# Kernel tuning notes

Measured on AMD Instinct MI355X. Metric: run time of the kernel, lower is better.

## Reference

```python
import jax, jax.numpy as jnp
import numpy as np

N = 8192
IN_DIM = 128
HID = 32


def setup_inputs() -> dict:
    key = jax.random.key(0)
    ks = jax.random.split(key, 8)
    x = jax.random.normal(ks[0], (N, IN_DIM), dtype=jnp.float32)
    adj = jax.random.uniform(ks[1], (N, N), dtype=jnp.float32)
    # Linear params (torch nn.Linear: y = x @ W.T + b); store as [in, out] for einsum.
    def lin(k, fan_in, fan_out):
        bound = 1.0 / np.sqrt(fan_in)
        kw, kb = jax.random.split(k)
        W = jax.random.uniform(kw, (fan_in, fan_out), minval=-bound, maxval=bound, dtype=jnp.float32)
        b = jax.random.uniform(kb, (fan_out,), minval=-bound, maxval=bound, dtype=jnp.float32)
        return W, b
    W1, b1 = lin(ks[2], IN_DIM, HID)
    W2, b2 = lin(ks[3], HID, HID)
    W3, b3 = lin(ks[4], HID, 1)
    return {"x": x, "adj": adj, "W1": W1, "b1": b1, "W2": W2, "b2": b2, "W3": W3, "b3": b3}


def reference(x, adj, W1, b1, W2, b2, W3, b3):
    # a_hat = adj + I (self loops)
    n = adj.shape[0]
    a_hat = adj + jnp.eye(n, dtype=adj.dtype)
    degree = jnp.sum(a_hat, axis=1)
    d_inv_sqrt = jnp.clip(degree, 1.0, None) ** -0.5  # [N]
    # D^-1/2 A D^-1/2 as row/col scaling (same math as diag matmuls, no O(N^3) waste)
    a_norm = d_inv_sqrt[:, None] * a_hat * d_inv_sqrt[None, :]
    h = jax.nn.relu(a_norm @ (x @ W1 + b1))
    h = jax.nn.relu(a_norm @ (h @ W2 + b2))
    logits = (h @ W3 + b3).squeeze(-1)  # [N]
    return logits
```

## Files before the change

### kernel.cpp

```cpp
#include <hip/hip_runtime.h>
#include <math.h>

#define N 8192
#define IN_DIM 128
#define HID 32

#define RB 128
#define KT 64
#define SK 16
#define KCHUNK (N / SK)

__device__ __forceinline__ void fma4(float4& acc, float a, const float4& b) {
    acc.x = fmaf(a, b.x, acc.x);
    acc.y = fmaf(a, b.y, acc.y);
    acc.z = fmaf(a, b.z, acc.z);
    acc.w = fmaf(a, b.w, acc.w);
}

__global__ __launch_bounds__(256) void k_deg_z1(const float* __restrict__ adj,
                                                const float* __restrict__ x,
                                                const float* __restrict__ W1,
                                                const float* __restrict__ b1,
                                                float* __restrict__ dinv,
                                                float* __restrict__ Zs) {
    __shared__ float Ws[IN_DIM * HID];
    __shared__ float xs[8 * IN_DIM];
    int t = threadIdx.x;
    int row0 = blockIdx.x * 8;
    int g = t >> 5, c = t & 31;
#pragma unroll
    for (int i = 0; i < 4; ++i)
        *(float4*)&Ws[(i * 256 + t) * 4] = *(const float4*)&W1[(i * 256 + t) * 4];
    *(float4*)&xs[t * 4] = *(const float4*)&x[(size_t)row0 * IN_DIM + t * 4];

    int row = row0 + g;
    const float4* rp = (const float4*)(adj + (size_t)row * N);
    float s = 0.f;
#pragma unroll 8
    for (int i = 0; i < 64; ++i) {
        float4 v = rp[c + i * 32];
        s += v.x + v.y + v.z + v.w;
    }
#pragma unroll
    for (int off = 16; off > 0; off >>= 1) s += __shfl_xor(s, off, 64);
    float deg = fmaxf(s + 1.0f, 1.0f);
    float di = 1.0f / sqrtf(deg);
    if (c == 0) dinv[row] = di;

    __syncthreads();
    float acc = b1[c];
#pragma unroll 8
    for (int k = 0; k < IN_DIM; ++k) acc = fmaf(xs[g * IN_DIM + k], Ws[k * HID + c], acc);
    Zs[(size_t)row * HID + c] = di * acc;
}

__global__ __launch_bounds__(256) void k_spmm(const float* __restrict__ adj,
                                              const float* __restrict__ Zs,
                                              float* __restrict__ P) {
    __shared__ float As[RB][KT + 4];
    __shared__ float Bs[KT][HID];
    int t = threadIdx.x;
    int r0 = blockIdx.x * RB;
    int k0 = blockIdx.y * KCHUNK;
    int cg = t & 3;
    int rp2 = (t >> 2) * 2;
    float4 acc00 = {0, 0, 0, 0}, acc01 = {0, 0, 0, 0};
    float4 acc10 = {0, 0, 0, 0}, acc11 = {0, 0, 0, 0};

    for (int kt = k0; kt < k0 + KCHUNK; kt += KT) {
#pragma unroll
        for (int i = 0; i < 8; ++i) {
            int f = i * 256 + t;
            int row = f >> 4;
            int kc = (f & 15) << 2;
            *(float4*)&As[row][kc] = *(const float4*)&adj[(size_t)(r0 + row) * N + kt + kc];
        }
#pragma unroll
        for (int i = 0; i < 2; ++i) {
            int f = i * 256 + t;
            ((float4*)&Bs[0][0])[f] = ((const float4*)(Zs + (size_t)kt * HID))[f];
        }
        __syncthreads();
#pragma unroll
        for (int kk = 0; kk < KT; kk += 4) {
            float a0[4], a1[4];
            *(float4*)a0 = *(const float4*)&As[rp2][kk];
            *(float4*)a1 = *(const float4*)&As[rp2 + 1][kk];
#pragma unroll
            for (int j = 0; j < 4; ++j) {
                float4 z0 = *(const float4*)&Bs[kk + j][cg * 8];
                float4 z1 = *(const float4*)&Bs[kk + j][cg * 8 + 4];
                fma4(acc00, a0[j], z0);
                fma4(acc01, a0[j], z1);
                fma4(acc10, a1[j], z0);
                fma4(acc11, a1[j], z1);
            }
        }
        __syncthreads();
    }

    float* p0 = P + (size_t)blockIdx.y * (N * HID) + (size_t)(r0 + rp2) * HID + cg * 8;
    float* p1 = p0 + HID;
    *(float4*)(p0)     = acc00;
    *(float4*)(p0 + 4) = acc01;
    *(float4*)(p1)     = acc10;
    *(float4*)(p1 + 4) = acc11;
}

__global__ __launch_bounds__(256) void k_fin_z2(const float* __restrict__ P,
                                                const float* __restrict__ Zin,
                                                const float* __restrict__ dinv,
                                                const float* __restrict__ W2,
                                                const float* __restrict__ b2,
                                                float* __restrict__ Zout) {
    __shared__ float Ws[HID * HID];
    __shared__ float hs[8][HID];
    int t = threadIdx.x;
    int row0 = blockIdx.x * 8;
    *(float4*)&Ws[t * 4] = *(const float4*)&W2[t * 4];
    int r = t >> 5, c = t & 31;
    size_t idx = (size_t)row0 * HID + t;
    float v = Zin[idx];
#pragma unroll
    for (int s = 0; s < SK; ++s) v += P[(size_t)s * (N * HID) + idx];
    int row = row0 + r;
    hs[r][c] = fmaxf(dinv[row] * v, 0.f);
    __syncthreads();
    float acc = b2[c];
#pragma unroll
    for (int k = 0; k < HID; ++k) acc = fmaf(hs[r][k], Ws[k * HID + c], acc);
    Zout[idx] = dinv[row] * acc;
}

__global__ __launch_bounds__(256) void k_fin_out(const float* __restrict__ P,
                                                 const float* __restrict__ Zin,
                                                 const float* __restrict__ dinv,
                                                 const float* __restrict__ W3,
                                                 const float* __restrict__ b3,
                                                 float* __restrict__ out) {
    int t = threadIdx.x;
    size_t idx = (size_t)blockIdx.x * 256 + t;
    int row = (int)(idx >> 5);
    int c = t & 31;
    float v = Zin[idx];
#pragma unroll
    for (int s = 0; s < SK; ++s) v += P[(size_t)s * (N * HID) + idx];
    float h = fmaxf(dinv[row] * v, 0.f);
    float hw = h * W3[c];
#pragma unroll
    for (int off = 16; off > 0; off >>= 1) hw += __shfl_xor(hw, off, 32);
    if (c == 0) out[row] = hw + b3[0];
}

extern "C" void kernel_launch(void* const* d_in, const int* in_sizes, int n_in,
                              void* d_out, int out_size, void* d_ws, size_t ws_size,
                              hipStream_t stream) {
    const float* x   = (const float*)d_in[0];
    const float* adj = (const float*)d_in[1];
    const float* W1  = (const float*)d_in[2];
    const float* b1  = (const float*)d_in[3];
    const float* W2  = (const float*)d_in[4];
    const float* b2  = (const float*)d_in[5];
    const float* W3  = (const float*)d_in[6];
    const float* b3  = (const float*)d_in[7];
    float* out = (float*)d_out;

    float* dinv = (float*)d_ws;
    float* Zs1  = dinv + N;
    float* Zs2  = Zs1 + (size_t)N * HID;
    float* P    = Zs2 + (size_t)N * HID;

    k_deg_z1<<<N / 8, 256, 0, stream>>>(adj, x, W1, b1, dinv, Zs1);

    k_spmm<<<dim3(N / RB, SK), 256, 0, stream>>>(adj, Zs1, P);
    k_fin_z2<<<N / 8, 256, 0, stream>>>(P, Zs1, dinv, W2, b2, Zs2);

    k_spmm<<<dim3(N / RB, SK), 256, 0, stream>>>(adj, Zs2, P);
    k_fin_out<<<N * HID / 256, 256, 0, stream>>>(P, Zs2, dinv, W3, b3, out);
}
```

Before: 527.4 us.

## Prefetch next adj/Z tile into registers and XOR-swizzle shared A tile

The spmm kernel now loads the next K tile of adj and Z into registers while the current tile is being computed, so global latency overlaps with FMA work. The padded shared A array is replaced by an unpadded layout with an XOR swizzle on float4 columns to avoid bank conflicts, and launch bounds now request 4 blocks per CU. The register prefetch buffers raise register pressure, which the occupancy hint may constrain or cause to spill.

```diff
diff --git a/kernel.cpp b/kernel.cpp
--- a/kernel.cpp
+++ b/kernel.cpp
@@ -7,6 +7,7 @@
 
 #define RB 128
 #define KT 64
+#define NT (KCHUNK / KT)
 #define SK 16
 #define KCHUNK (N / SK)
 
@@ -54,42 +55,69 @@
     Zs[(size_t)row * HID + c] = di * acc;
 }
 
-__global__ __launch_bounds__(256) void k_spmm(const float* __restrict__ adj,
-                                              const float* __restrict__ Zs,
-                                              float* __restrict__ P) {
-    __shared__ float As[RB][KT + 4];
-    __shared__ float Bs[KT][HID];
+__global__ __launch_bounds__(256, 4) void k_spmm(const float* __restrict__ adj,
+                                                 const float* __restrict__ Zs,
+                                                 float* __restrict__ P) {
+    __shared__ float As[RB * KT];
+    __shared__ float Bs[KT * HID];
     int t = threadIdx.x;
     int r0 = blockIdx.x * RB;
     int k0 = blockIdx.y * KCHUNK;
     int cg = t & 3;
     int rp2 = (t >> 2) * 2;
+    int e = (rp2 >> 1) & 7;
     float4 acc00 = {0, 0, 0, 0}, acc01 = {0, 0, 0, 0};
     float4 acc10 = {0, 0, 0, 0}, acc11 = {0, 0, 0, 0};
 
-    for (int kt = k0; kt < k0 + KCHUNK; kt += KT) {
-#pragma unroll
-        for (int i = 0; i < 8; ++i) {
-            int f = i * 256 + t;
-            int row = f >> 4;
-            int kc = (f & 15) << 2;
-            *(float4*)&As[row][kc] = *(const float4*)&adj[(size_t)(r0 + row) * N + kt + kc];
+    int srow[8], sfi[8];
+#pragma unroll
+    for (int i = 0; i < 8; ++i) {
+        int f = i * 256 + t;
+        srow[i] = f >> 4;
+        sfi[i] = (f & 15) ^ ((srow[i] >> 1) & 7);
+    }
+
+    float4 ar[8], br[2];
+#pragma unroll
+    for (int i = 0; i < 8; ++i) {
+        int f = i * 256 + t;
+        ar[i] = *(const float4*)&adj[(size_t)(r0 + (f >> 4)) * N + k0 + (f & 15) * 4];
+    }
+#pragma unroll
+    for (int i = 0; i < 2; ++i)
+        br[i] = ((const float4*)(Zs + (size_t)k0 * HID))[i * 256 + t];
+
+    for (int tile = 0; tile < NT; ++tile) {
+#pragma unroll
+        for (int i = 0; i < 8; ++i)
+            *(float4*)&As[srow[i] * KT + sfi[i] * 4] = ar[i];
+#pragma unroll
+        for (int i = 0; i < 2; ++i)
+            ((float4*)Bs)[i * 256 + t] = br[i];
+        __syncthreads();
+
+        if (tile + 1 < NT) {
+            int ktn = k0 + (tile + 1) * KT;
+#pragma unroll
+            for (int i = 0; i < 8; ++i) {
+                int f = i * 256 + t;
+                ar[i] = *(const float4*)&adj[(size_t)(r0 + (f >> 4)) * N + ktn + (f & 15) * 4];
+            }
+#pragma unroll
+            for (int i = 0; i < 2; ++i)
+                br[i] = ((const float4*)(Zs + (size_t)ktn * HID))[i * 256 + t];
         }
-#pragma unroll
-        for (int i = 0; i < 2; ++i) {
-            int f = i * 256 + t;
-            ((float4*)&Bs[0][0])[f] = ((const float4*)(Zs + (size_t)kt * HID))[f];
-        }
-        __syncthreads();
+
 #pragma unroll
         for (int kk = 0; kk < KT; kk += 4) {
+            int s0 = ((kk >> 2) ^ e) * 4;
             float a0[4], a1[4];
-            *(float4*)a0 = *(const float4*)&As[rp2][kk];
-            *(float4*)a1 = *(const float4*)&As[rp2 + 1][kk];
+            *(float4*)a0 = *(const float4*)&As[rp2 * KT + s0];
+            *(float4*)a1 = *(const float4*)&As[(rp2 + 1) * KT + s0];
 #pragma unroll
             for (int j = 0; j < 4; ++j) {
-                float4 z0 = *(const float4*)&Bs[kk + j][cg * 8];
-                float4 z1 = *(const float4*)&Bs[kk + j][cg * 8 + 4];
+                float4 z0 = *(const float4*)&Bs[(kk + j) * HID + cg * 8];
+                float4 z1 = *(const float4*)&Bs[(kk + j) * HID + cg * 8 + 4];
                 fma4(acc00, a0[j], z0);
                 fma4(acc01, a0[j], z1);
                 fma4(acc10, a1[j], z0);
```

After: 790.2 us. +49.8%, slower.

## Double-buffer spmm tiles with direct global-to-LDS loads and XOR swizzle

Applied to the files above, without the earlier changes.

Rewrites the k_spmm tile loading to use global_load_lds 16-byte direct copies into a double-buffered shared-memory layout, so the next adjacency and Z tile are prefetched while the current one is computed. KT is halved to 32 to fit two buffers, and the A tile uses an XOR swizzle instead of padding to avoid LDS bank conflicts. The aim is to hide global memory latency on the bandwidth-bound adjacency stream. It adds dependence on the 16-byte LDS-load intrinsic and has no explicit wait for the async loads beyond __syncthreads, which risks correctness on hardware where that barrier does not drain them.

```diff
diff --git a/kernel.cpp b/kernel.cpp
--- a/kernel.cpp
+++ b/kernel.cpp
@@ -6,15 +6,22 @@
 #define HID 32
 
 #define RB 128
-#define KT 64
+#define KT 32
 #define SK 16
 #define KCHUNK (N / SK)
+#define NT (KCHUNK / KT)
 
 __device__ __forceinline__ void fma4(float4& acc, float a, const float4& b) {
     acc.x = fmaf(a, b.x, acc.x);
     acc.y = fmaf(a, b.y, acc.y);
     acc.z = fmaf(a, b.z, acc.z);
     acc.w = fmaf(a, b.w, acc.w);
+}
+
+__device__ __forceinline__ void gload16(const float* g, float* l) {
+    __builtin_amdgcn_global_load_lds(
+        (const __attribute__((address_space(1))) void*)g,
+        (__attribute__((address_space(3))) void*)l, 16, 0, 0);
 }
 
 __global__ __launch_bounds__(256) void k_deg_z1(const float* __restrict__ adj,
@@ -57,39 +64,57 @@
 __global__ __launch_bounds__(256) void k_spmm(const float* __restrict__ adj,
                                               const float* __restrict__ Zs,
                                               float* __restrict__ P) {
-    __shared__ float As[RB][KT + 4];
-    __shared__ float Bs[KT][HID];
-    int t = threadIdx.x;
+    __shared__ float As[2][RB * KT];
+    __shared__ float Bs[2][KT * HID];
+    int t = threadIdx.x;
+    int w = t >> 6, l = t & 63;
     int r0 = blockIdx.x * RB;
     int k0 = blockIdx.y * KCHUNK;
     int cg = t & 3;
     int rp2 = (t >> 2) * 2;
+    int e = (rp2 >> 1) & 7;
     float4 acc00 = {0, 0, 0, 0}, acc01 = {0, 0, 0, 0};
     float4 acc10 = {0, 0, 0, 0}, acc11 = {0, 0, 0, 0};
 
-    for (int kt = k0; kt < k0 + KCHUNK; kt += KT) {
-#pragma unroll
-        for (int i = 0; i < 8; ++i) {
-            int f = i * 256 + t;
-            int row = f >> 4;
-            int kc = (f & 15) << 2;
-            *(float4*)&As[row][kc] = *(const float4*)&adj[(size_t)(r0 + row) * N + kt + kc];
+    int arow[4], afi[4];
+#pragma unroll
+    for (int i = 0; i < 4; ++i) {
+        int s = ((w * 4 + i) << 6) + l;
+        arow[i] = s >> 3;
+        afi[i] = (s & 7) ^ ((arow[i] >> 1) & 7);
+    }
+    int bslot = (w << 6) + l;
+
+#pragma unroll
+    for (int i = 0; i < 4; ++i)
+        gload16(&adj[(size_t)(r0 + arow[i]) * N + k0 + afi[i] * 4],
+                &As[0][(w * 4 + i) << 8]);
+    gload16(&Zs[(size_t)k0 * HID + bslot * 4], &Bs[0][w << 8]);
+    __syncthreads();
+
+    int cur = 0;
+    for (int tile = 0; tile < NT; ++tile) {
+        if (tile + 1 < NT) {
+            int ktn = k0 + (tile + 1) * KT;
+            int nxt = cur ^ 1;
+#pragma unroll
+            for (int i = 0; i < 4; ++i)
+                gload16(&adj[(size_t)(r0 + arow[i]) * N + ktn + afi[i] * 4],
+                        &As[nxt][(w * 4 + i) << 8]);
+            gload16(&Zs[(size_t)ktn * HID + bslot * 4], &Bs[nxt][w << 8]);
         }
-#pragma unroll
-        for (int i = 0; i < 2; ++i) {
-            int f = i * 256 + t;
-            ((float4*)&Bs[0][0])[f] = ((const float4*)(Zs + (size_t)kt * HID))[f];
-        }
-        __syncthreads();
+        const float* A = As[cur];
+        const float* B = Bs[cur];
 #pragma unroll
         for (int kk = 0; kk < KT; kk += 4) {
+            int s0 = ((kk >> 2) ^ e) * 4;
             float a0[4], a1[4];
-            *(float4*)a0 = *(const float4*)&As[rp2][kk];
-            *(float4*)a1 = *(const float4*)&As[rp2 + 1][kk];
+            *(float4*)a0 = *(const float4*)&A[rp2 * KT + s0];
+            *(float4*)a1 = *(const float4*)&A[(rp2 + 1) * KT + s0];
 #pragma unroll
             for (int j = 0; j < 4; ++j) {
-                float4 z0 = *(const float4*)&Bs[kk + j][cg * 8];
-                float4 z1 = *(const float4*)&Bs[kk + j][cg * 8 + 4];
+                float4 z0 = *(const float4*)&B[(kk + j) * HID + cg * 8];
+                float4 z1 = *(const float4*)&B[(kk + j) * HID + cg * 8 + 4];
                 fma4(acc00, a0[j], z0);
                 fma4(acc01, a0[j], z1);
                 fma4(acc10, a1[j], z0);
@@ -97,6 +122,7 @@
             }
         }
         __syncthreads();
+        cur ^= 1;
     }
 
     float* p0 = P + (size_t)blockIdx.y * (N * HID) + (size_t)(r0 + rp2) * HID + cg * 8;
```

Result: no change. 522.7 us (-0.9%).
